# Kernel tuning notes

Hardware: AMD Instinct MI355X
Metric: run time of the kernel (lower is better)

Reference implementation:

```python
import jax, jax.numpy as jnp
import numpy as np

N0, N1, N2, N3 = 200000, 50000, 12000, 3000
E0, E1, E2 = 500000, 120000, 30000
D_IN, D_H, D_OUT = 256, 256, 64


def setup_inputs() -> dict:
    key = jax.random.key(0)
    ks = jax.random.split(key, 16)
    s = 1.0 / np.sqrt(D_IN)
    return {
        "x": jax.random.normal(ks[0], (N0, D_IN), jnp.float32),
        "src0": jax.random.randint(ks[1], (E0,), 0, N0),
        "dst0": jax.random.randint(ks[2], (E0,), 0, N1),
        "src1": jax.random.randint(ks[3], (E1,), 0, N1),
        "dst1": jax.random.randint(ks[4], (E1,), 0, N2),
        "src2": jax.random.randint(ks[5], (E2,), 0, N2),
        "dst2": jax.random.randint(ks[6], (E2,), 0, N3),
        "num_dst0": N1, "num_dst1": N2, "num_dst2": N3,
        "Ws0": jax.random.normal(ks[7], (D_IN, D_H), jnp.float32) * s,
        "Wn0": jax.random.normal(ks[8], (D_IN, D_H), jnp.float32) * s,
        "b0": jnp.zeros((D_H,), jnp.float32),
        "Ws1": jax.random.normal(ks[9], (D_H, D_H), jnp.float32) * s,
        "Wn1": jax.random.normal(ks[10], (D_H, D_H), jnp.float32) * s,
        "b1": jnp.zeros((D_H,), jnp.float32),
        "Ws2": jax.random.normal(ks[11], (D_H, D_OUT), jnp.float32) * s,
        "Wn2": jax.random.normal(ks[12], (D_H, D_OUT), jnp.float32) * s,
        "b2": jnp.zeros((D_OUT,), jnp.float32),
    }


def sage_conv(src, dst, num_dst, h_src, Wn, Ws, b):
    # DGL SAGEConv(mean): fc_self(h_dst) + fc_neigh(mean_{in-edges} h_src) + bias
    h_dst = h_src[:num_dst]
    msg = h_src[src]                                          # [E, d] gather
    agg = jax.ops.segment_sum(msg, dst, num_segments=num_dst)  # [num_dst, d]
    deg = jax.ops.segment_sum(jnp.ones((dst.shape[0],), h_src.dtype), dst,
                              num_segments=num_dst)
    h_neigh = agg / jnp.maximum(deg, 1.0)[:, None]
    return h_dst @ Ws + h_neigh @ Wn + b


def reference(x, src0, dst0, src1, dst1, src2, dst2,
              num_dst0, num_dst1, num_dst2,
              Ws0, Wn0, b0, Ws1, Wn1, b1, Ws2, Wn2, b2):
    h = sage_conv(src0, dst0, num_dst0, x, Wn0, Ws0, b0)       # layer 0 (no act, per source)
    h = sage_conv(src1, dst1, num_dst1, h, Wn1, Ws1, b1)       # layer 1
    h = jax.nn.relu(h)                                         # activation after middle layer
    # dropout omitted (eval / deterministic mode)
    h = sage_conv(src2, dst2, num_dst2, h, Wn2, Ws2, b2)       # layer 2
    return h
```

## Files before the change

### kernel.cpp

```cpp
#include <hip/hip_runtime.h>

#define N0_SRC 200000
#define N1_DST 50000
#define N2_DST 12000
#define N3_DST 3000
#define NTOT_DST 65000
#define DH 256
#define DOUT 64
#define EMAX_TOT 650000

typedef __attribute__((ext_vector_type(8))) short short8;
typedef __attribute__((ext_vector_type(4))) float f32x4;

__device__ __forceinline__ ushort f2bf(float f) {
    union { float f; uint32_t u; } v; v.f = f;
    uint32_t r = (v.u + 0x7FFF + ((v.u >> 16) & 1)) >> 16;
    return (ushort)r;
}
__device__ __forceinline__ float bf2f(ushort u) {
    union { uint32_t u; float f; } v; v.u = ((uint32_t)u) << 16;
    return v.f;
}

__global__ void f32_to_bf16_kernel(const float* __restrict__ in,
                                   ushort* __restrict__ out, long n) {
    long i = ((long)blockIdx.x * 256 + threadIdx.x) * 4;
    if (i >= n) return;
    float4 v = *(const float4*)(in + i);
    ushort4 o;
    o.x = f2bf(v.x); o.y = f2bf(v.y); o.z = f2bf(v.z); o.w = f2bf(v.w);
    *(ushort4*)(out + i) = o;
}

__global__ void transpose_w_all(const float* __restrict__ W0, const float* __restrict__ W1,
                                const float* __restrict__ W2, const float* __restrict__ W3,
                                const float* __restrict__ W4, const float* __restrict__ W5,
                                ushort* __restrict__ out) {
    const float* W; int Ndim; ushort* o;
    switch (blockIdx.y) {
        case 0: W = W0; Ndim = 256; o = out; break;
        case 1: W = W1; Ndim = 256; o = out + 65536; break;
        case 2: W = W2; Ndim = 256; o = out + 131072; break;
        case 3: W = W3; Ndim = 256; o = out + 196608; break;
        case 4: W = W4; Ndim = 64;  o = out + 262144; break;
        default: W = W5; Ndim = 64; o = out + 278528; break;
    }
    int id = blockIdx.x * 256 + threadIdx.x;
    int n = id >> 8;
    int k = id & 255;
    if (n >= Ndim) return;
    o[id] = f2bf(W[k * Ndim + n]);
}

__global__ void hist3_kernel(const int* __restrict__ d0, int E0,
                             const int* __restrict__ d1, int E1,
                             const int* __restrict__ d2, int E2,
                             int* __restrict__ cnt) {
    int layer = blockIdx.y;
    const int* dst; int E; int base;
    if (layer == 0)      { dst = d0; E = E0; base = 0; }
    else if (layer == 1) { dst = d1; E = E1; base = N1_DST; }
    else                 { dst = d2; E = E2; base = N1_DST + N2_DST; }
    int e = blockIdx.x * 256 + threadIdx.x;
    if (e < E) atomicAdd(&cnt[base + dst[e]], 1);
}

__global__ void fill3_kernel(const int* __restrict__ s0, const int* __restrict__ d0, int E0,
                             const int* __restrict__ s1, const int* __restrict__ d1, int E1,
                             const int* __restrict__ s2, const int* __restrict__ d2, int E2,
                             int* __restrict__ cursor, int* __restrict__ eidx) {
    int layer = blockIdx.y;
    const int* src; const int* dst; int E; int base;
    if (layer == 0)      { src = s0; dst = d0; E = E0; base = 0; }
    else if (layer == 1) { src = s1; dst = d1; E = E1; base = N1_DST; }
    else                 { src = s2; dst = d2; E = E2; base = N1_DST + N2_DST; }
    int e = blockIdx.x * 256 + threadIdx.x;
    if (e < E) {
        int p = atomicAdd(&cursor[base + dst[e]], 1);
        eidx[p] = src[e];
    }
}

__global__ void scan_phase_a(const int* __restrict__ cnt, int* __restrict__ partial, int n) {
    __shared__ int red[4];
    int t = threadIdx.x;
    int i = blockIdx.x * 1024 + t * 4;
    int s = 0;
    if (i + 3 < n) {
        int4 v = *(const int4*)(cnt + i);
        s = v.x + v.y + v.z + v.w;
    }
#pragma unroll
    for (int d = 32; d; d >>= 1) s += __shfl_down(s, d, 64);
    if ((t & 63) == 0) red[t >> 6] = s;
    __syncthreads();
    if (t == 0) partial[blockIdx.x] = red[0] + red[1] + red[2] + red[3];
}

__global__ void scan_phase_b(int* __restrict__ partial, int nb) {
    int t = threadIdx.x;
    int own = (t < nb) ? partial[t] : 0;
    int v = own;
#pragma unroll
    for (int d = 1; d < 64; d <<= 1) {
        int u = __shfl_up(v, d, 64);
        if (t >= d) v += u;
    }
    if (t < nb) partial[t] = v - own;
}

__global__ void scan_phase_c(const int* __restrict__ cnt, const int* __restrict__ partial,
                             int* __restrict__ off, int* __restrict__ cursor, int n) {
    __shared__ int tsum[256];
    int t = threadIdx.x;
    int i = blockIdx.x * 1024 + t * 4;
    int4 c = make_int4(0, 0, 0, 0);
    if (i + 3 < n) c = *(const int4*)(cnt + i);
    int s = c.x + c.y + c.z + c.w;
    tsum[t] = s;
    __syncthreads();
#pragma unroll
    for (int d = 1; d < 256; d <<= 1) {
        int u = (t >= d) ? tsum[t - d] : 0;
        __syncthreads();
        tsum[t] += u;
        __syncthreads();
    }
    int base = partial[blockIdx.x] + tsum[t] - s;
    if (i + 3 < n) {
        int4 ov;
        ov.x = base;
        ov.y = ov.x + c.x;
        ov.z = ov.y + c.y;
        ov.w = ov.z + c.z;
        *(int4*)(off + i) = ov;
        *(int4*)(cursor + i) = ov;
        if (i + 4 == n) off[n] = ov.w + c.w;
    }
}

__global__ void gather_mean_bf16_kernel(const ushort* __restrict__ h,
                                        const int* __restrict__ off,
                                        const int* __restrict__ eidx,
                                        ushort* __restrict__ hn,
                                        int num_dst) {
    int w = blockIdx.x * 4 + (threadIdx.x >> 6);
    int lane = threadIdx.x & 63;
    if (w >= num_dst) return;
    int beg = off[w];
    int end = off[w + 1];
    float a0 = 0.f, a1 = 0.f, a2 = 0.f, a3 = 0.f;
    int i = beg;
    for (; i + 3 < end; i += 4) {
        int s0 = eidx[i], s1 = eidx[i + 1], s2 = eidx[i + 2], s3 = eidx[i + 3];
        ushort4 v0 = ((const ushort4*)(h + (size_t)s0 * DH))[lane];
        ushort4 v1 = ((const ushort4*)(h + (size_t)s1 * DH))[lane];
        ushort4 v2 = ((const ushort4*)(h + (size_t)s2 * DH))[lane];
        ushort4 v3 = ((const ushort4*)(h + (size_t)s3 * DH))[lane];
        a0 += (bf2f(v0.x) + bf2f(v1.x)) + (bf2f(v2.x) + bf2f(v3.x));
        a1 += (bf2f(v0.y) + bf2f(v1.y)) + (bf2f(v2.y) + bf2f(v3.y));
        a2 += (bf2f(v0.z) + bf2f(v1.z)) + (bf2f(v2.z) + bf2f(v3.z));
        a3 += (bf2f(v0.w) + bf2f(v1.w)) + (bf2f(v2.w) + bf2f(v3.w));
    }
    for (; i < end; ++i) {
        int s0 = eidx[i];
        ushort4 v0 = ((const ushort4*)(h + (size_t)s0 * DH))[lane];
        a0 += bf2f(v0.x); a1 += bf2f(v0.y); a2 += bf2f(v0.z); a3 += bf2f(v0.w);
    }
    float inv = 1.0f / fmaxf((float)(end - beg), 1.0f);
    ushort4 o;
    o.x = f2bf(a0 * inv); o.y = f2bf(a1 * inv);
    o.z = f2bf(a2 * inv); o.w = f2bf(a3 * inv);
    *(ushort4*)(hn + (size_t)w * DH + lane * 4) = o;
}

template <int BN, bool RELU, bool OUT_BF16>
__global__ void gemm_mfma(const ushort* __restrict__ Ad,
                          const ushort* __restrict__ An,
                          const ushort* __restrict__ Wst,
                          const ushort* __restrict__ Wnt,
                          const float* __restrict__ bias,
                          void* __restrict__ Cv,
                          int M, int N) {
    const int K = 256;
    const int LDK = 40;
    const int NT = BN / 16;
    __shared__ ushort As[128 * LDK];
    __shared__ ushort Bs[BN * LDK];

    int tid  = threadIdx.x;
    int lane = tid & 63;
    int wid  = tid >> 6;
    int quad = lane >> 4;
    int mr   = lane & 15;
    int row0 = blockIdx.y * 128;
    int col0 = blockIdx.x * BN;

    f32x4 acc[2][NT];
#pragma unroll
    for (int i = 0; i < 2; ++i)
#pragma unroll
        for (int j = 0; j < NT; ++j) acc[i][j] = (f32x4){0.f, 0.f, 0.f, 0.f};

    for (int pass = 0; pass < 2; ++pass) {
        const ushort* A  = pass ? An : Ad;
        const ushort* Wt = pass ? Wnt : Wst;
        for (int k0 = 0; k0 < K; k0 += 32) {
#pragma unroll
            for (int c = 0; c < 2; ++c) {
                int chunk = tid + c * 256;
                int r   = chunk >> 2;
                int seg = chunk & 3;
                int row = row0 + r;
                uint4 v = make_uint4(0u, 0u, 0u, 0u);
                if (row < M) v = *(const uint4*)(A + (size_t)row * K + k0 + seg * 8);
                *(uint4*)(&As[r * LDK + seg * 8]) = v;
            }
#pragma unroll
            for (int c = 0; c < BN / 64; ++c) {
                int chunk = tid + c * 256;
                int n   = chunk >> 2;
                int seg = chunk & 3;
                uint4 v = *(const uint4*)(Wt + (size_t)(col0 + n) * K + k0 + seg * 8);
                *(uint4*)(&Bs[n * LDK + seg * 8]) = v;
            }
            __syncthreads();
            short8 a[2], b[NT];
#pragma unroll
            for (int mt = 0; mt < 2; ++mt)
                a[mt] = *(const short8*)(&As[(wid * 32 + mt * 16 + mr) * LDK + quad * 8]);
#pragma unroll
            for (int nt = 0; nt < NT; ++nt)
                b[nt] = *(const short8*)(&Bs[(nt * 16 + mr) * LDK + quad * 8]);
#pragma unroll
            for (int mt = 0; mt < 2; ++mt)
#pragma unroll
                for (int nt = 0; nt < NT; ++nt)
                    acc[mt][nt] = __builtin_amdgcn_mfma_f32_16x16x32_bf16(
                        a[mt], b[nt], acc[mt][nt], 0, 0, 0);
            __syncthreads();
        }
    }

#pragma unroll
    for (int mt = 0; mt < 2; ++mt) {
#pragma unroll
        for (int i = 0; i < 4; ++i) {
            int row = row0 + wid * 32 + mt * 16 + quad * 4 + i;
            if (row >= M) continue;
#pragma unroll
            for (int nt = 0; nt < NT; ++nt) {
                int col = col0 + nt * 16 + mr;
                float v = acc[mt][nt][i] + bias[col];
                if (RELU) v = fmaxf(v, 0.0f);
                if (OUT_BF16) ((ushort*)Cv)[(size_t)row * N + col] = f2bf(v);
                else          ((float*)Cv)[(size_t)row * N + col] = v;
            }
        }
    }
}

extern "C" void kernel_launch(void* const* d_in, const int* in_sizes, int n_in,
                              void* d_out, int out_size, void* d_ws, size_t ws_size,
                              hipStream_t stream) {
    const float* x    = (const float*)d_in[0];
    const int* src0   = (const int*)d_in[1];
    const int* dst0   = (const int*)d_in[2];
    const int* src1   = (const int*)d_in[3];
    const int* dst1   = (const int*)d_in[4];
    const int* src2   = (const int*)d_in[5];
    const int* dst2   = (const int*)d_in[6];
    const float* Ws0  = (const float*)d_in[10];
    const float* Wn0  = (const float*)d_in[11];
    const float* b0   = (const float*)d_in[12];
    const float* Ws1  = (const float*)d_in[13];
    const float* Wn1  = (const float*)d_in[14];
    const float* b1   = (const float*)d_in[15];
    const float* Ws2  = (const float*)d_in[16];
    const float* Wn2  = (const float*)d_in[17];
    const float* b2   = (const float*)d_in[18];
    float* out = (float*)d_out;

    int E0 = in_sizes[1];
    int E1 = in_sizes[3];
    int E2 = in_sizes[5];

    ushort* wsu  = (ushort*)d_ws;
    ushort* xb   = wsu;
    ushort* hn0b = xb   + (size_t)N0_SRC * DH;
    ushort* h1b  = hn0b + (size_t)N1_DST * DH;
    ushort* hn1b = h1b  + (size_t)N1_DST * DH;
    ushort* h2b  = hn1b + (size_t)N2_DST * DH;
    ushort* hn2b = h2b  + (size_t)N2_DST * DH;
    ushort* Wt   = hn2b + (size_t)N3_DST * DH;
    ushort* Ws0t = Wt;
    ushort* Wn0t = Wt + 65536;
    ushort* Ws1t = Wt + 131072;
    ushort* Wn1t = Wt + 196608;
    ushort* Ws2t = Wt + 262144;
    ushort* Wn2t = Wt + 278528;
    int* cnt     = (int*)(Wt + 294912);
    int* off     = cnt + NTOT_DST;
    int* cursor  = off + NTOT_DST + 4;
    int* eidx    = cursor + NTOT_DST;
    int* partial = eidx + EMAX_TOT;

    long nxb = (long)N0_SRC * DH;
    f32_to_bf16_kernel<<<(int)((nxb / 4 + 255) / 256), 256, 0, stream>>>(x, xb, nxb);
    transpose_w_all<<<dim3(256, 6), 256, 0, stream>>>(Ws0, Wn0, Ws1, Wn1, Ws2, Wn2, Wt);

    int Emax = max(max(E0, E1), E2);
    int nb = (NTOT_DST + 1023) / 1024;
    hipMemsetAsync(cnt, 0, NTOT_DST * sizeof(int), stream);
    hist3_kernel<<<dim3((Emax + 255) / 256, 3), 256, 0, stream>>>(dst0, E0, dst1, E1, dst2, E2, cnt);
    scan_phase_a<<<nb, 256, 0, stream>>>(cnt, partial, NTOT_DST);
    scan_phase_b<<<1, 64, 0, stream>>>(partial, nb);
    scan_phase_c<<<nb, 256, 0, stream>>>(cnt, partial, off, cursor, NTOT_DST);
    fill3_kernel<<<dim3((Emax + 255) / 256, 3), 256, 0, stream>>>(
        src0, dst0, E0, src1, dst1, E1, src2, dst2, E2, cursor, eidx);

    const int* off0 = off;
    const int* off1 = off + N1_DST;
    const int* off2 = off + N1_DST + N2_DST;

    gather_mean_bf16_kernel<<<(N1_DST + 3) / 4, 256, 0, stream>>>(xb, off0, eidx, hn0b, N1_DST);
    {
        dim3 g(DH / 128, (N1_DST + 127) / 128);
        gemm_mfma<128, false, true><<<g, 256, 0, stream>>>(xb, hn0b, Ws0t, Wn0t, b0, h1b, N1_DST, DH);
    }

    gather_mean_bf16_kernel<<<(N2_DST + 3) / 4, 256, 0, stream>>>(h1b, off1, eidx, hn1b, N2_DST);
    {
        dim3 g(DH / 128, (N2_DST + 127) / 128);
        gemm_mfma<128, true, true><<<g, 256, 0, stream>>>(h1b, hn1b, Ws1t, Wn1t, b1, h2b, N2_DST, DH);
    }

    gather_mean_bf16_kernel<<<(N3_DST + 3) / 4, 256, 0, stream>>>(h2b, off2, eidx, hn2b, N3_DST);
    {
        dim3 g(DOUT / 64, (N3_DST + 127) / 128);
        gemm_mfma<64, false, false><<<g, 256, 0, stream>>>(h2b, hn2b, Ws2t, Wn2t, b2, out, N3_DST, DOUT);
    }
}
```

Baseline: 523.5 us.

## Fuse prep kernels into one launch and enlarge GEMM K-tile and warp tiles

Merges the fp32-to-bf16 conversion, the weight transpose and the degree histogram into one kernel that dispatches on block index, cutting launches and letting the three independent jobs run concurrently. Separately, the MFMA GEMM now stages a K-tile of 64 instead of 32, halving barriers per pass. For BN=128 it gives each wave a 64x64 sub-tile, which raises register use for accumulators. The larger shared tiles and accumulator count may reduce occupancy.

```diff
diff --git a/kernel.cpp b/kernel.cpp
--- a/kernel.cpp
+++ b/kernel.cpp
@@ -22,47 +22,113 @@
     return v.f;
 }
 
-__global__ void f32_to_bf16_kernel(const float* __restrict__ in,
-                                   ushort* __restrict__ out, long n) {
-    long i = ((long)blockIdx.x * 256 + threadIdx.x) * 4;
-    if (i >= n) return;
-    float4 v = *(const float4*)(in + i);
-    ushort4 o;
-    o.x = f2bf(v.x); o.y = f2bf(v.y); o.z = f2bf(v.z); o.w = f2bf(v.w);
-    *(ushort4*)(out + i) = o;
-}
-
-__global__ void transpose_w_all(const float* __restrict__ W0, const float* __restrict__ W1,
-                                const float* __restrict__ W2, const float* __restrict__ W3,
-                                const float* __restrict__ W4, const float* __restrict__ W5,
-                                ushort* __restrict__ out) {
-    const float* W; int Ndim; ushort* o;
-    switch (blockIdx.y) {
-        case 0: W = W0; Ndim = 256; o = out; break;
-        case 1: W = W1; Ndim = 256; o = out + 65536; break;
-        case 2: W = W2; Ndim = 256; o = out + 131072; break;
-        case 3: W = W3; Ndim = 256; o = out + 196608; break;
-        case 4: W = W4; Ndim = 64;  o = out + 262144; break;
-        default: W = W5; Ndim = 64; o = out + 278528; break;
-    }
-    int id = blockIdx.x * 256 + threadIdx.x;
-    int n = id >> 8;
-    int k = id & 255;
-    if (n >= Ndim) return;
-    o[id] = f2bf(W[k * Ndim + n]);
-}
-
-__global__ void hist3_kernel(const int* __restrict__ d0, int E0,
-                             const int* __restrict__ d1, int E1,
-                             const int* __restrict__ d2, int E2,
-                             int* __restrict__ cnt) {
-    int layer = blockIdx.y;
+#define CONV_BLOCKS (N0_SRC * DH / 1024)
+#define TRANS_BLOCKS 1536
+
+__global__ void mega_prep_kernel(const float* __restrict__ x, ushort* __restrict__ xb,
+                                 const float* __restrict__ W0, const float* __restrict__ W1,
+                                 const float* __restrict__ W2, const float* __restrict__ W3,
+                                 const float* __restrict__ W4, const float* __restrict__ W5,
+                                 ushort* __restrict__ Wt,
+                                 const int* __restrict__ d0, int E0,
+                                 const int* __restrict__ d1, int E1,
+                                 const int* __restrict__ d2, int E2,
+                                 int hb0, int hb1,
+                                 int* __restrict__ cnt) {
+    int bid = blockIdx.x;
+    int tid = threadIdx.x;
+    if (bid < CONV_BLOCKS) {
+        long i = ((long)bid * 256 + tid) * 4;
+        float4 v = *(const float4*)(x + i);
+        ushort4 o;
+        o.x = f2bf(v.x); o.y = f2bf(v.y); o.z = f2bf(v.z); o.w = f2bf(v.w);
+        *(ushort4*)(xb + i) = o;
+        return;
+    }
+    bid -= CONV_BLOCKS;
+    if (bid < TRANS_BLOCKS) {
+        int wsel = bid >> 8;
+        int blk  = bid & 255;
+        const float* W; int Ndim; ushort* o;
+        switch (wsel) {
+            case 0: W = W0; Ndim = 256; o = Wt; break;
+            case 1: W = W1; Ndim = 256; o = Wt + 65536; break;
+            case 2: W = W2; Ndim = 256; o = Wt + 131072; break;
+            case 3: W = W3; Ndim = 256; o = Wt + 196608; break;
+            case 4: W = W4; Ndim = 64;  o = Wt + 262144; break;
+            default: W = W5; Ndim = 64; o = Wt + 278528; break;
+        }
+        int id = blk * 256 + tid;
+        int n = id >> 8;
+        int k = id & 255;
+        if (n < Ndim) o[id] = f2bf(W[k * Ndim + n]);
+        return;
+    }
+    bid -= TRANS_BLOCKS;
     const int* dst; int E; int base;
-    if (layer == 0)      { dst = d0; E = E0; base = 0; }
-    else if (layer == 1) { dst = d1; E = E1; base = N1_DST; }
-    else                 { dst = d2; E = E2; base = N1_DST + N2_DST; }
-    int e = blockIdx.x * 256 + threadIdx.x;
+    if (bid < hb0)            { dst = d0; E = E0; base = 0; }
+    else if (bid < hb0 + hb1) { dst = d1; E = E1; base = N1_DST; bid -= hb0; }
+    else                      { dst = d2; E = E2; base = N1_DST + N2_DST; bid -= hb0 + hb1; }
+    int e = bid * 256 + tid;
     if (e < E) atomicAdd(&cnt[base + dst[e]], 1);
+}
+
+__global__ void scan_phase_a(const int* __restrict__ cnt, int* __restrict__ partial, int n) {
+    __shared__ int red[4];
+    int t = threadIdx.x;
+    int i = blockIdx.x * 1024 + t * 4;
+    int s = 0;
+    if (i + 3 < n) {
+        int4 v = *(const int4*)(cnt + i);
+        s = v.x + v.y + v.z + v.w;
+    }
+#pragma unroll
+    for (int d = 32; d; d >>= 1) s += __shfl_down(s, d, 64);
+    if ((t & 63) == 0) red[t >> 6] = s;
+    __syncthreads();
+    if (t == 0) partial[blockIdx.x] = red[0] + red[1] + red[2] + red[3];
+}
+
+__global__ void scan_phase_b(int* __restrict__ partial, int nb) {
+    int t = threadIdx.x;
+    int own = (t < nb) ? partial[t] : 0;
+    int v = own;
+#pragma unroll
+    for (int d = 1; d < 64; d <<= 1) {
+        int u = __shfl_up(v, d, 64);
+        if (t >= d) v += u;
+    }
+    if (t < nb) partial[t] = v - own;
+}
+
+__global__ void scan_phase_c(const int* __restrict__ cnt, const int* __restrict__ partial,
+                             int* __restrict__ off, int* __restrict__ cursor, int n) {
+    __shared__ int tsum[256];
+    int t = threadIdx.x;
+    int i = blockIdx.x * 1024 + t * 4;
+    int4 c = make_int4(0, 0, 0, 0);
+    if (i + 3 < n) c = *(const int4*)(cnt + i);
+    int s = c.x + c.y + c.z + c.w;
+    tsum[t] = s;
+    __syncthreads();
+#pragma unroll
+    for (int d = 1; d < 256; d <<= 1) {
+        int u = (t >= d) ? tsum[t - d] : 0;
+        __syncthreads();
+        tsum[t] += u;
+        __syncthreads();
+    }
+    int base = partial[blockIdx.x] + tsum[t] - s;
+    if (i + 3 < n) {
+        int4 ov;
+        ov.x = base;
+        ov.y = ov.x + c.x;
+        ov.z = ov.y + c.y;
+        ov.w = ov.z + c.z;
+        *(int4*)(off + i) = ov;
+        *(int4*)(cursor + i) = ov;
+        if (i + 4 == n) off[n] = ov.w + c.w;
+    }
 }
 
 __global__ void fill3_kernel(const int* __restrict__ s0, const int* __restrict__ d0, int E0,
@@ -78,64 +144,6 @@
     if (e < E) {
         int p = atomicAdd(&cursor[base + dst[e]], 1);
         eidx[p] = src[e];
-    }
-}
-
-__global__ void scan_phase_a(const int* __restrict__ cnt, int* __restrict__ partial, int n) {
-    __shared__ int red[4];
-    int t = threadIdx.x;
-    int i = blockIdx.x * 1024 + t * 4;
-    int s = 0;
-    if (i + 3 < n) {
-        int4 v = *(const int4*)(cnt + i);
-        s = v.x + v.y + v.z + v.w;
-    }
-#pragma unroll
-    for (int d = 32; d; d >>= 1) s += __shfl_down(s, d, 64);
-    if ((t & 63) == 0) red[t >> 6] = s;
-    __syncthreads();
-    if (t == 0) partial[blockIdx.x] = red[0] + red[1] + red[2] + red[3];
-}
-
-__global__ void scan_phase_b(int* __restrict__ partial, int nb) {
-    int t = threadIdx.x;
-    int own = (t < nb) ? partial[t] : 0;
-    int v = own;
-#pragma unroll
-    for (int d = 1; d < 64; d <<= 1) {
-        int u = __shfl_up(v, d, 64);
-        if (t >= d) v += u;
-    }
-    if (t < nb) partial[t] = v - own;
-}
-
-__global__ void scan_phase_c(const int* __restrict__ cnt, const int* __restrict__ partial,
-                             int* __restrict__ off, int* __restrict__ cursor, int n) {
-    __shared__ int tsum[256];
-    int t = threadIdx.x;
-    int i = blockIdx.x * 1024 + t * 4;
-    int4 c = make_int4(0, 0, 0, 0);
-    if (i + 3 < n) c = *(const int4*)(cnt + i);
-    int s = c.x + c.y + c.z + c.w;
-    tsum[t] = s;
-    __syncthreads();
-#pragma unroll
-    for (int d = 1; d < 256; d <<= 1) {
-        int u = (t >= d) ? tsum[t - d] : 0;
-        __syncthreads();
-        tsum[t] += u;
-        __syncthreads();
-    }
-    int base = partial[blockIdx.x] + tsum[t] - s;
-    if (i + 3 < n) {
-        int4 ov;
-        ov.x = base;
-        ov.y = ov.x + c.x;
-        ov.z = ov.y + c.y;
-        ov.w = ov.z + c.z;
-        *(int4*)(off + i) = ov;
-        *(int4*)(cursor + i) = ov;
-        if (i + 4 == n) off[n] = ov.w + c.w;
     }
 }
 
@@ -183,8 +191,10 @@
                           void* __restrict__ Cv,
                           int M, int N) {
     const int K = 256;
-    const int LDK = 40;
-    const int NT = BN / 16;
+    const int BK = 64;
+    const int LDK = 72;
+    const int MT = (BN == 128) ? 4 : 2;
+    const int NT = 4;
     __shared__ ushort As[128 * LDK];
     __shared__ ushort Bs[BN * LDK];
 
@@ -195,62 +205,67 @@
     int mr   = lane & 15;
     int row0 = blockIdx.y * 128;
     int col0 = blockIdx.x * BN;
-
-    f32x4 acc[2][NT];
-#pragma unroll
-    for (int i = 0; i < 2; ++i)
+    int wm   = (BN == 128) ? (wid >> 1) * 64 : wid * 32;
+    int wn   = (BN == 128) ? (wid & 1) * 64 : 0;
+
+    f32x4 acc[MT][NT];
+#pragma unroll
+    for (int i = 0; i < MT; ++i)
 #pragma unroll
         for (int j = 0; j < NT; ++j) acc[i][j] = (f32x4){0.f, 0.f, 0.f, 0.f};
 
     for (int pass = 0; pass < 2; ++pass) {
         const ushort* A  = pass ? An : Ad;
         const ushort* Wt = pass ? Wnt : Wst;
-        for (int k0 = 0; k0 < K; k0 += 32) {
-#pragma unroll
-            for (int c = 0; c < 2; ++c) {
+        for (int k0 = 0; k0 < K; k0 += BK) {
+#pragma unroll
+            for (int c = 0; c < 4; ++c) {
                 int chunk = tid + c * 256;
-                int r   = chunk >> 2;
-                int seg = chunk & 3;
+                int r   = chunk >> 3;
+                int seg = chunk & 7;
                 int row = row0 + r;
                 uint4 v = make_uint4(0u, 0u, 0u, 0u);
                 if (row < M) v = *(const uint4*)(A + (size_t)row * K + k0 + seg * 8);
                 *(uint4*)(&As[r * LDK + seg * 8]) = v;
             }
 #pragma unroll
-            for (int c = 0; c < BN / 64; ++c) {
+            for (int c = 0; c < BN / 32; ++c) {
                 int chunk = tid + c * 256;
-                int n   = chunk >> 2;
-                int seg = chunk & 3;
+                int n   = chunk >> 3;
+                int seg = chunk & 7;
                 uint4 v = *(const uint4*)(Wt + (size_t)(col0 + n) * K + k0 + seg * 8);
                 *(uint4*)(&Bs[n * LDK + seg * 8]) = v;
             }
             __syncthreads();
-            short8 a[2], b[NT];
-#pragma unroll
-            for (int mt = 0; mt < 2; ++mt)
-                a[mt] = *(const short8*)(&As[(wid * 32 + mt * 16 + mr) * LDK + quad * 8]);
-#pragma unroll
-            for (int nt = 0; nt < NT; ++nt)
-                b[nt] = *(const short8*)(&Bs[(nt * 16 + mr) * LDK + quad * 8]);
-#pragma unroll
-            for (int mt = 0; mt < 2; ++mt)
+#pragma unroll
+            for (int ks = 0; ks < BK; ks += 32) {
+                short8 a[MT], b[NT];
+#pragma unroll
+                for (int mt = 0; mt < MT; ++mt)
+                    a[mt] = *(const short8*)(&As[(wm + mt * 16 + mr) * LDK + ks + quad * 8]);
 #pragma unroll
                 for (int nt = 0; nt < NT; ++nt)
-                    acc[mt][nt] = __builtin_amdgcn_mfma_f32_16x16x32_bf16(
-                        a[mt], b[nt], acc[mt][nt], 0, 0, 0);
+                    b[nt] = *(const short8*)(&Bs[(wn + nt * 16 + mr) * LDK + ks + quad * 8]);
+#pragma unroll
+                for (int mt = 0; mt < MT; ++mt)
+#pragma unroll
+                    for (int nt = 0; nt < NT; ++nt)
+                        acc[mt][nt] = __builtin_amdgcn_mfma_f32_16x16x32_bf16(
+                            a[mt], b[nt], acc[mt][nt], 0, 0, 0);
+            }
             __syncthreads();
         }
     }
 
 #pragma unroll
-    for (int mt = 0; mt < 2; ++mt) {
+    for (int mt = 0; mt < MT; ++mt) {
 #pragma unroll
         for (int i = 0; i < 4; ++i) {
-            int row = row0 + wid * 32 + mt * 16 + quad * 4 + i;
+            int row = row0 + wm + mt * 16 + quad * 4 + i;
             if (row >= M) continue;
 #pragma unroll
             for (int nt = 0; nt < NT; ++nt) {
-                int col = col0 + nt * 16 + mr;
+                int col = col0 + wn + nt * 16 + mr;
                 float v = acc[mt][nt][i] + bias[col];
                 if (RELU) v = fmaxf(v, 0.0f);
                 if (OUT_BF16) ((ushort*)Cv)[(size_t)row * N + col] = f2bf(v);
@@ -305,17 +320,20 @@
     int* eidx    = cursor + NTOT_DST;
     int* partial = eidx + EMAX_TOT;
 
-    long nxb = (long)N0_SRC * DH;
-    f32_to_bf16_kernel<<<(int)((nxb / 4 + 255) / 256), 256, 0, stream>>>(x, xb, nxb);
-    transpose_w_all<<<dim3(256, 6), 256, 0, stream>>>(Ws0, Wn0, Ws1, Wn1, Ws2, Wn2, Wt);
-
-    int Emax = max(max(E0, E1), E2);
+    int hb0 = (E0 + 255) / 256;
+    int hb1 = (E1 + 255) / 256;
+    int hb2 = (E2 + 255) / 256;
+    hipMemsetAsync(cnt, 0, NTOT_DST * sizeof(int), stream);
+    int mega_blocks = CONV_BLOCKS + TRANS_BLOCKS + hb0 + hb1 + hb2;
+    mega_prep_kernel<<<mega_blocks, 256, 0, stream>>>(
+        x, xb, Ws0, Wn0, Ws1, Wn1, Ws2, Wn2, Wt,
+        dst0, E0, dst1, E1, dst2, E2, hb0, hb1, cnt);
+
     int nb = (NTOT_DST + 1023) / 1024;
-    hipMemsetAsync(cnt, 0, NTOT_DST * sizeof(int), stream);
-    hist3_kernel<<<dim3((Emax + 255) / 256, 3), 256, 0, stream>>>(dst0, E0, dst1, E1, dst2, E2, cnt);
     scan_phase_a<<<nb, 256, 0, stream>>>(cnt, partial, NTOT_DST);
     scan_phase_b<<<1, 64, 0, stream>>>(partial, nb);
     scan_phase_c<<<nb, 256, 0, stream>>>(cnt, partial, off, cursor, NTOT_DST);
+    int Emax = max(max(E0, E1), E2);
     fill3_kernel<<<dim3((Emax + 255) / 256, 3), 256, 0, stream>>>(
         src0, dst0, E0, src1, dst1, E1, src2, dst2, E2, cursor, eidx);
 
```

Result: slower. 562.7 us (+7.5%).
